# Kernel optimization log

Measured on AMD Instinct MI355X. Metric: run time of the kernel, lower is better.

Reference implementation:

```python
import jax, jax.numpy as jnp
import numpy as np

B, T, D, H = 128, 1024, 128, 512

def setup_inputs() -> dict:
    key = jax.random.key(0)
    ks = jax.random.split(key, 7)
    s = 1.0 / np.sqrt(H)
    return {
        "x":    jax.random.normal(ks[0], (B, T, D), dtype=jnp.float32),
        "W_ih": jax.random.uniform(ks[1], (4 * H, D), jnp.float32, -s, s),
        "W_hh": jax.random.uniform(ks[2], (4 * H, H), jnp.float32, -s, s),
        "b_ih": jax.random.uniform(ks[3], (4 * H,), jnp.float32, -s, s),
        "b_hh": jax.random.uniform(ks[4], (4 * H,), jnp.float32, -s, s),
        "W_fc": jax.random.uniform(ks[5], (1, H), jnp.float32, -s, s),
        "b_fc": jax.random.uniform(ks[6], (1,), jnp.float32, -s, s),
    }

def _lstm_last_hidden(x, W_ih, W_hh, b_ih, b_hh):
    # Precompute input-side gate projections for all timesteps: [T, B, 4H]
    xg = jnp.einsum('btd,gd->tbg', x, W_ih) + (b_ih + b_hh)
    Bq = x.shape[0]
    Hq = W_hh.shape[1]
    h0 = jnp.zeros((Bq, Hq), x.dtype)
    c0 = jnp.zeros((Bq, Hq), x.dtype)

    def step(carry, g_in):
        h, c = carry
        g = g_in + h @ W_hh.T                      # [B, 4H]
        i, f, gc, o = jnp.split(g, 4, axis=-1)     # PyTorch gate order i,f,g,o
        i = jax.nn.sigmoid(i)
        f = jax.nn.sigmoid(f)
        gc = jnp.tanh(gc)
        o = jax.nn.sigmoid(o)
        c = f * c + i * gc
        h = o * jnp.tanh(c)
        return (h, c), None

    (h_last, _), _ = jax.lax.scan(step, (h0, c0), xg)
    return h_last

def reference(x, W_ih, W_hh, b_ih, b_hh, W_fc, b_fc):
    h = _lstm_last_hidden(x, W_ih, W_hh, b_ih, b_hh)   # out[:, -1, :]
    return jax.nn.sigmoid(h @ W_fc.T + b_fc)           # [B, 1]
```

## Files before the change

kernel.cpp:

```cpp
#include <hip/hip_runtime.h>
#include <hip/hip_bf16.h>

#define Bsz 128
#define Tsz 1024
#define Dsz 128
#define Hsz 512
#define NBLK 256
#define NKC 20

typedef __attribute__((ext_vector_type(8))) short short8;
typedef __attribute__((ext_vector_type(4))) float f4;
typedef unsigned long long u64;

__device__ __forceinline__ short bf16_rne(float f) {
  unsigned u = __builtin_bit_cast(unsigned, f);
  u += 0x7fffu + ((u >> 16) & 1u);
  return (short)(u >> 16);
}
__device__ __forceinline__ float sigmoid_(float v) { return 1.f / (1.f + __expf(-v)); }

__global__ __launch_bounds__(256, 1) void lstm_persist(
    const float* __restrict__ x, const float* __restrict__ W_ih,
    const float* __restrict__ W_hh, const float* __restrict__ b_ih,
    const float* __restrict__ b_hh, const float* __restrict__ W_fc,
    const float* __restrict__ b_fc, float* __restrict__ out,
    int* flags, unsigned short* hb0, unsigned short* hb1)
{
  const int bx = blockIdx.x;
  const int bt = bx & 7, ks = bx >> 3;
  const int b0 = bt << 4, k0 = ks << 4;
  const int tx = threadIdx.x;
  const int wave = tx >> 6, lane = tx & 63;
  const int m = lane & 15, quad = lane >> 4;
  const int k_l = tx & 15, b_l = tx >> 4;

  __shared__ short8 A_lds[NKC][64];
  __shared__ f4 gates_lds[4][64];
  __shared__ float fc_red[16][16];

  int* gflags = flags + bt * 32;

  short8 wfrag[NKC];
  {
    const int j = wave * Hsz + k0 + m;
    #pragma unroll
    for (int kc = 0; kc < NKC; ++kc) {
      const int kk = kc * 32 + quad * 8;
      const float* src = (kk < Dsz) ? (W_ih + (size_t)j * Dsz + kk)
                                    : (W_hh + (size_t)j * Hsz + (kk - Dsz));
      const f4* sv = (const f4*)src;
      f4 v0 = sv[0], v1 = sv[1];
      short8 w;
      w[0] = bf16_rne(v0[0]); w[1] = bf16_rne(v0[1]);
      w[2] = bf16_rne(v0[2]); w[3] = bf16_rne(v0[3]);
      w[4] = bf16_rne(v1[0]); w[5] = bf16_rne(v1[1]);
      w[6] = bf16_rne(v1[2]); w[7] = bf16_rne(v1[3]);
      wfrag[kc] = w;
    }
  }
  float bias[4];
  #pragma unroll
  for (int g = 0; g < 4; ++g)
    bias[g] = b_ih[g * Hsz + k0 + k_l] + b_hh[g * Hsz + k0 + k_l];
  float c_reg = 0.f;

  for (int t = 0; t < Tsz; ++t) {
    unsigned short* hnext = (t & 1) ? hb1 : hb0;
    const unsigned short* hprev = (t & 1) ? hb0 : hb1;

    const f4* xv = (const f4*)(x + (size_t)(b0 + m) * (Tsz * Dsz)
                               + (size_t)t * Dsz + wave * 32 + quad * 8);
    f4 v0 = xv[0], v1 = xv[1];

    if (t > 0) {
      for (;;) {
        int f = __hip_atomic_load(gflags + (lane & 31),
                                  __ATOMIC_RELAXED, __HIP_MEMORY_SCOPE_AGENT);
        if (__all(f >= t)) break;
        __builtin_amdgcn_s_sleep(1);
      }
      #pragma unroll
      for (int q = 0; q < 4; ++q) {
        const int kc = 4 + wave * 4 + q;
        const int kh = (kc - 4) * 32 + quad * 8;
        const u64* p = (const u64*)(hprev + (size_t)(b0 + m) * Hsz + kh);
        u64 lo = __hip_atomic_load(p,     __ATOMIC_RELAXED, __HIP_MEMORY_SCOPE_AGENT);
        u64 hi = __hip_atomic_load(p + 1, __ATOMIC_RELAXED, __HIP_MEMORY_SCOPE_AGENT);
        u64* dst = (u64*)&A_lds[kc][lane];
        dst[0] = lo; dst[1] = hi;
      }
    } else {
      short8 z = {0, 0, 0, 0, 0, 0, 0, 0};
      #pragma unroll
      for (int q = 0; q < 4; ++q) A_lds[4 + wave * 4 + q][lane] = z;
    }

    {
      short8 a;
      a[0] = bf16_rne(v0[0]); a[1] = bf16_rne(v0[1]);
      a[2] = bf16_rne(v0[2]); a[3] = bf16_rne(v0[3]);
      a[4] = bf16_rne(v1[0]); a[5] = bf16_rne(v1[1]);
      a[6] = bf16_rne(v1[2]); a[7] = bf16_rne(v1[3]);
      A_lds[wave][lane] = a;
    }
    __syncthreads();

    f4 acc0 = {0.f, 0.f, 0.f, 0.f}, acc1 = {0.f, 0.f, 0.f, 0.f};
    #pragma unroll
    for (int kc = 0; kc < NKC; kc += 2) {
      acc0 = __builtin_amdgcn_mfma_f32_16x16x32_bf16(A_lds[kc][lane],     wfrag[kc],     acc0, 0, 0, 0);
      acc1 = __builtin_amdgcn_mfma_f32_16x16x32_bf16(A_lds[kc + 1][lane], wfrag[kc + 1], acc1, 0, 0, 0);
    }
    gates_lds[wave][lane] = acc0 + acc1;
    __syncthreads();

    {
      const int lp = ((b_l >> 2) << 4) + k_l;
      const int r = b_l & 3;
      float pi = gates_lds[0][lp][r] + bias[0];
      float pf = gates_lds[1][lp][r] + bias[1];
      float pg = gates_lds[2][lp][r] + bias[2];
      float po = gates_lds[3][lp][r] + bias[3];
      float iv = sigmoid_(pi), fv = sigmoid_(pf), ov = sigmoid_(po);
      float gv = tanhf(pg);
      c_reg = fv * c_reg + iv * gv;
      float hv = ov * tanhf(c_reg);
      unsigned hbits = (unsigned)(unsigned short)bf16_rne(hv);
      unsigned obits = __shfl_xor(hbits, 1);
      if ((k_l & 1) == 0) {
        unsigned packed = hbits | (obits << 16);
        unsigned* p = (unsigned*)(hnext + (size_t)(b0 + b_l) * Hsz + k0 + k_l);
        __hip_atomic_store(p, packed, __ATOMIC_RELAXED, __HIP_MEMORY_SCOPE_AGENT);
      }
    }
    __syncthreads();
    if (tx == 0)
      __hip_atomic_store(gflags + ks, t + 1, __ATOMIC_RELAXED, __HIP_MEMORY_SCOPE_AGENT);
  }

  if (ks == 0) {
    for (;;) {
      int f = __hip_atomic_load(gflags + (lane & 31),
                                __ATOMIC_RELAXED, __HIP_MEMORY_SCOPE_AGENT);
      if (__all(f >= Tsz)) break;
      __builtin_amdgcn_s_sleep(1);
    }
    const unsigned short* hl = hb1;
    const u64* p = (const u64*)(hl + (size_t)(b0 + b_l) * Hsz + k_l * 32);
    float partial = 0.f;
    #pragma unroll
    for (int q = 0; q < 8; ++q) {
      u64 v = __hip_atomic_load(p + q, __ATOMIC_RELAXED, __HIP_MEMORY_SCOPE_AGENT);
      #pragma unroll
      for (int e = 0; e < 4; ++e) {
        unsigned hv16 = (unsigned)((v >> (16 * e)) & 0xffffu);
        partial += __builtin_bit_cast(float, hv16 << 16) * W_fc[k_l * 32 + q * 4 + e];
      }
    }
    fc_red[b_l][k_l] = partial;
    __syncthreads();
    if (k_l == 0) {
      float s = b_fc[0];
      #pragma unroll
      for (int e = 0; e < 16; ++e) s += fc_red[b_l][e];
      out[b0 + b_l] = sigmoid_(s);
    }
  }
}

extern "C" void kernel_launch(void* const* d_in, const int* in_sizes, int n_in,
                              void* d_out, int out_size, void* d_ws, size_t ws_size,
                              hipStream_t stream) {
  const float* x    = (const float*)d_in[0];
  const float* W_ih = (const float*)d_in[1];
  const float* W_hh = (const float*)d_in[2];
  const float* b_ih = (const float*)d_in[3];
  const float* b_hh = (const float*)d_in[4];
  const float* W_fc = (const float*)d_in[5];
  const float* b_fc = (const float*)d_in[6];
  float* out = (float*)d_out;
  char* ws = (char*)d_ws;
  int* flags = (int*)ws;
  unsigned short* hb0 = (unsigned short*)(ws + 4096);
  unsigned short* hb1 = (unsigned short*)(ws + 4096 + (size_t)Bsz * Hsz * 2);
  hipMemsetAsync(ws, 0, 4096, stream);
  lstm_persist<<<NBLK, 256, 0, stream>>>(x, W_ih, W_hh, b_ih, b_hh, W_fc, b_fc,
                                         out, flags, hb0, hb1);
}
```

Baseline: 3.124 ms.

## Restructure LSTM step: gate-interleaved weights, shuffle gate exchange, padded flags, x prefetch

```diff
diff --git a/kernel.cpp b/kernel.cpp
--- a/kernel.cpp
+++ b/kernel.cpp
@@ -6,18 +6,24 @@
 #define Dsz 128
 #define Hsz 512
 #define NBLK 256
-#define NKC 20
+#define NXC 4
+#define NHC 16
 
 typedef __attribute__((ext_vector_type(8))) short short8;
 typedef __attribute__((ext_vector_type(4))) float f4;
 typedef unsigned long long u64;
 
-__device__ __forceinline__ short bf16_rne(float f) {
+__device__ __forceinline__ unsigned short bf16_rne(float f) {
   unsigned u = __builtin_bit_cast(unsigned, f);
   u += 0x7fffu + ((u >> 16) & 1u);
-  return (short)(u >> 16);
+  return (unsigned short)(u >> 16);
 }
 __device__ __forceinline__ float sigmoid_(float v) { return 1.f / (1.f + __expf(-v)); }
+__device__ __forceinline__ float tanh_(float v) {
+  v = fminf(fmaxf(v, -15.f), 15.f);
+  float e = __expf(2.f * v);
+  return (e - 1.f) / (e + 1.f);
+}
 
 __global__ __launch_bounds__(256, 1) void lstm_persist(
     const float* __restrict__ x, const float* __restrict__ W_ih,
@@ -32,19 +38,22 @@
   const int tx = threadIdx.x;
   const int wave = tx >> 6, lane = tx & 63;
   const int m = lane & 15, quad = lane >> 4;
-  const int k_l = tx & 15, b_l = tx >> 4;
-
-  __shared__ short8 A_lds[NKC][64];
-  __shared__ f4 gates_lds[4][64];
+  const int g_own = (lane >> 2) & 3, c_own = lane & 3;
+  const int mycol = k0 + wave * 4 + c_own;
+  const int myrow = b0 + quad * 4 + g_own;
+
+  __shared__ short8 A_x[2][NXC][64];
+  __shared__ short8 A_h[NHC][64];
   __shared__ float fc_red[16][16];
-
-  int* gflags = flags + bt * 32;
-
-  short8 wfrag[NKC];
+  __shared__ int token;
+
+  int* gflags = flags + bt * 1024;
+
+  short8 wfrag[NXC + NHC];
   {
-    const int j = wave * Hsz + k0 + m;
-    #pragma unroll
-    for (int kc = 0; kc < NKC; ++kc) {
+    const int j = g_own * Hsz + k0 + wave * 4 + c_own;
+    #pragma unroll
+    for (int kc = 0; kc < NXC + NHC; ++kc) {
       const int kk = kc * 32 + quad * 8;
       const float* src = (kk < Dsz) ? (W_ih + (size_t)j * Dsz + kk)
                                     : (W_hh + (size_t)j * Hsz + (kk - Dsz));
@@ -58,95 +67,127 @@
       wfrag[kc] = w;
     }
   }
-  float bias[4];
-  #pragma unroll
-  for (int g = 0; g < 4; ++g)
-    bias[g] = b_ih[g * Hsz + k0 + k_l] + b_hh[g * Hsz + k0 + k_l];
+  const float bias0 = b_ih[0 * Hsz + mycol] + b_hh[0 * Hsz + mycol];
+  const float bias1 = b_ih[1 * Hsz + mycol] + b_hh[1 * Hsz + mycol];
+  const float bias2 = b_ih[2 * Hsz + mycol] + b_hh[2 * Hsz + mycol];
+  const float bias3 = b_ih[3 * Hsz + mycol] + b_hh[3 * Hsz + mycol];
   float c_reg = 0.f;
+
+  {
+    const f4* xv = (const f4*)(x + (size_t)(b0 + m) * (Tsz * Dsz) + wave * 32 + quad * 8);
+    f4 v0 = xv[0], v1 = xv[1];
+    short8 a;
+    a[0] = bf16_rne(v0[0]); a[1] = bf16_rne(v0[1]);
+    a[2] = bf16_rne(v0[2]); a[3] = bf16_rne(v0[3]);
+    a[4] = bf16_rne(v1[0]); a[5] = bf16_rne(v1[1]);
+    a[6] = bf16_rne(v1[2]); a[7] = bf16_rne(v1[3]);
+    A_x[0][wave][lane] = a;
+    short8 z = {0, 0, 0, 0, 0, 0, 0, 0};
+    #pragma unroll
+    for (int q = 0; q < 4; ++q) A_h[wave * 4 + q][lane] = z;
+    if (tx == 0) token = 0;
+  }
 
   for (int t = 0; t < Tsz; ++t) {
     unsigned short* hnext = (t & 1) ? hb1 : hb0;
     const unsigned short* hprev = (t & 1) ? hb0 : hb1;
 
-    const f4* xv = (const f4*)(x + (size_t)(b0 + m) * (Tsz * Dsz)
-                               + (size_t)t * Dsz + wave * 32 + quad * 8);
-    f4 v0 = xv[0], v1 = xv[1];
-
     if (t > 0) {
-      for (;;) {
-        int f = __hip_atomic_load(gflags + (lane & 31),
-                                  __ATOMIC_RELAXED, __HIP_MEMORY_SCOPE_AGENT);
-        if (__all(f >= t)) break;
-        __builtin_amdgcn_s_sleep(1);
+      if (wave == 0) {
+        const int fi = (lane & 31) * 32;
+        for (;;) {
+          int f = __hip_atomic_load(gflags + fi, __ATOMIC_RELAXED, __HIP_MEMORY_SCOPE_AGENT);
+          if (__all(f >= t)) break;
+          __builtin_amdgcn_s_sleep(1);
+        }
+        __hip_atomic_store(&token, t, __ATOMIC_RELAXED, __HIP_MEMORY_SCOPE_WORKGROUP);
+      } else {
+        while (__hip_atomic_load(&token, __ATOMIC_RELAXED, __HIP_MEMORY_SCOPE_WORKGROUP) < t) {}
       }
       #pragma unroll
       for (int q = 0; q < 4; ++q) {
-        const int kc = 4 + wave * 4 + q;
-        const int kh = (kc - 4) * 32 + quad * 8;
-        const u64* p = (const u64*)(hprev + (size_t)(b0 + m) * Hsz + kh);
+        const int hc = wave * 4 + q;
+        const u64* p = (const u64*)(hprev + (size_t)(b0 + m) * Hsz + hc * 32 + quad * 8);
         u64 lo = __hip_atomic_load(p,     __ATOMIC_RELAXED, __HIP_MEMORY_SCOPE_AGENT);
         u64 hi = __hip_atomic_load(p + 1, __ATOMIC_RELAXED, __HIP_MEMORY_SCOPE_AGENT);
-        u64* dst = (u64*)&A_lds[kc][lane];
+        u64* dst = (u64*)&A_h[hc][lane];
         dst[0] = lo; dst[1] = hi;
       }
-    } else {
-      short8 z = {0, 0, 0, 0, 0, 0, 0, 0};
-      #pragma unroll
-      for (int q = 0; q < 4; ++q) A_lds[4 + wave * 4 + q][lane] = z;
-    }
-
-    {
+    }
+    __syncthreads();
+
+    const int xb = t & 1;
+    f4 acc0 = {0.f, 0.f, 0.f, 0.f}, acc1 = {0.f, 0.f, 0.f, 0.f};
+    acc0 = __builtin_amdgcn_mfma_f32_16x16x32_bf16(A_x[xb][0][lane], wfrag[0], acc0, 0, 0, 0);
+    acc1 = __builtin_amdgcn_mfma_f32_16x16x32_bf16(A_x[xb][1][lane], wfrag[1], acc1, 0, 0, 0);
+    acc0 = __builtin_amdgcn_mfma_f32_16x16x32_bf16(A_x[xb][2][lane], wfrag[2], acc0, 0, 0, 0);
+    acc1 = __builtin_amdgcn_mfma_f32_16x16x32_bf16(A_x[xb][3][lane], wfrag[3], acc1, 0, 0, 0);
+    #pragma unroll
+    for (int hc = 0; hc < NHC; hc += 2) {
+      acc0 = __builtin_amdgcn_mfma_f32_16x16x32_bf16(A_h[hc][lane],     wfrag[NXC + hc],     acc0, 0, 0, 0);
+      acc1 = __builtin_amdgcn_mfma_f32_16x16x32_bf16(A_h[hc + 1][lane], wfrag[NXC + hc + 1], acc1, 0, 0, 0);
+    }
+    f4 acc = acc0 + acc1;
+
+    float a01 = (g_own & 1) ? acc[1] : acc[0];
+    float a23 = (g_own & 1) ? acc[3] : acc[2];
+    float own = (g_own & 2) ? a23 : a01;
+    float b01 = (g_own & 1) ? acc[0] : acc[1];
+    float b23 = (g_own & 1) ? acc[2] : acc[3];
+    float s1 = (g_own & 2) ? b23 : b01;
+    float s2 = (g_own & 2) ? a01 : a23;
+    float s3 = (g_own & 2) ? b01 : b23;
+    float x4  = __shfl_xor(s1, 4);
+    float x8  = __shfl_xor(s2, 8);
+    float x12 = __shfl_xor(s3, 12);
+    #define PICK(e) ({ int _e = (e); float _lo = (_e & 1) ? x4 : own; \
+                       float _hi = (_e & 1) ? x12 : x8; (_e & 2) ? _hi : _lo; })
+    float pi = PICK(g_own)     + bias0;
+    float pf = PICK(g_own ^ 1) + bias1;
+    float pg = PICK(g_own ^ 2) + bias2;
+    float po = PICK(g_own ^ 3) + bias3;
+    #undef PICK
+    float iv = sigmoid_(pi), fv = sigmoid_(pf), ov = sigmoid_(po);
+    float gv = tanh_(pg);
+    c_reg = fv * c_reg + iv * gv;
+    float hv = ov * tanh_(c_reg);
+
+    float h1 = __shfl_xor(hv, 1);
+    float h2 = __shfl_xor(hv, 2);
+    float h3 = __shfl_xor(hv, 3);
+    if (c_own == 0) {
+      u64 packed = (u64)bf16_rne(hv) | ((u64)bf16_rne(h1) << 16)
+                 | ((u64)bf16_rne(h2) << 32) | ((u64)bf16_rne(h3) << 48);
+      u64* p = (u64*)(hnext + (size_t)myrow * Hsz + k0 + wave * 4);
+      __hip_atomic_store(p, packed, __ATOMIC_RELAXED, __HIP_MEMORY_SCOPE_AGENT);
+    }
+
+    if (t + 1 < Tsz) {
+      const f4* xv = (const f4*)(x + (size_t)(b0 + m) * (Tsz * Dsz)
+                                 + (size_t)(t + 1) * Dsz + wave * 32 + quad * 8);
+      f4 v0 = xv[0], v1 = xv[1];
       short8 a;
       a[0] = bf16_rne(v0[0]); a[1] = bf16_rne(v0[1]);
       a[2] = bf16_rne(v0[2]); a[3] = bf16_rne(v0[3]);
       a[4] = bf16_rne(v1[0]); a[5] = bf16_rne(v1[1]);
       a[6] = bf16_rne(v1[2]); a[7] = bf16_rne(v1[3]);
-      A_lds[wave][lane] = a;
-    }
-    __syncthreads();
-
-    f4 acc0 = {0.f, 0.f, 0.f, 0.f}, acc1 = {0.f, 0.f, 0.f, 0.f};
-    #pragma unroll
-    for (int kc = 0; kc < NKC; kc += 2) {
-      acc0 = __builtin_amdgcn_mfma_f32_16x16x32_bf16(A_lds[kc][lane],     wfrag[kc],     acc0, 0, 0, 0);
-      acc1 = __builtin_amdgcn_mfma_f32_16x16x32_bf16(A_lds[kc + 1][lane], wfrag[kc + 1], acc1, 0, 0, 0);
-    }
-    gates_lds[wave][lane] = acc0 + acc1;
-    __syncthreads();
-
-    {
-      const int lp = ((b_l >> 2) << 4) + k_l;
-      const int r = b_l & 3;
-      float pi = gates_lds[0][lp][r] + bias[0];
-      float pf = gates_lds[1][lp][r] + bias[1];
-      float pg = gates_lds[2][lp][r] + bias[2];
-      float po = gates_lds[3][lp][r] + bias[3];
-      float iv = sigmoid_(pi), fv = sigmoid_(pf), ov = sigmoid_(po);
-      float gv = tanhf(pg);
-      c_reg = fv * c_reg + iv * gv;
-      float hv = ov * tanhf(c_reg);
-      unsigned hbits = (unsigned)(unsigned short)bf16_rne(hv);
-      unsigned obits = __shfl_xor(hbits, 1);
-      if ((k_l & 1) == 0) {
-        unsigned packed = hbits | (obits << 16);
-        unsigned* p = (unsigned*)(hnext + (size_t)(b0 + b_l) * Hsz + k0 + k_l);
-        __hip_atomic_store(p, packed, __ATOMIC_RELAXED, __HIP_MEMORY_SCOPE_AGENT);
-      }
-    }
+      A_x[(t + 1) & 1][wave][lane] = a;
+    }
+
     __syncthreads();
     if (tx == 0)
-      __hip_atomic_store(gflags + ks, t + 1, __ATOMIC_RELAXED, __HIP_MEMORY_SCOPE_AGENT);
+      __hip_atomic_store(gflags + ks * 32, t + 1, __ATOMIC_RELAXED, __HIP_MEMORY_SCOPE_AGENT);
   }
 
   if (ks == 0) {
+    const int k_l = tx & 15, b_l = tx >> 4;
+    const int fi = (lane & 31) * 32;
     for (;;) {
-      int f = __hip_atomic_load(gflags + (lane & 31),
-                                __ATOMIC_RELAXED, __HIP_MEMORY_SCOPE_AGENT);
+      int f = __hip_atomic_load(gflags + fi, __ATOMIC_RELAXED, __HIP_MEMORY_SCOPE_AGENT);
       if (__all(f >= Tsz)) break;
       __builtin_amdgcn_s_sleep(1);
     }
-    const unsigned short* hl = hb1;
-    const u64* p = (const u64*)(hl + (size_t)(b0 + b_l) * Hsz + k_l * 32);
+    const u64* p = (const u64*)(hb1 + (size_t)(b0 + b_l) * Hsz + k_l * 32);
     float partial = 0.f;
     #pragma unroll
     for (int q = 0; q < 8; ++q) {
@@ -181,9 +222,9 @@
   float* out = (float*)d_out;
   char* ws = (char*)d_ws;
   int* flags = (int*)ws;
-  unsigned short* hb0 = (unsigned short*)(ws + 4096);
-  unsigned short* hb1 = (unsigned short*)(ws + 4096 + (size_t)Bsz * Hsz * 2);
-  hipMemsetAsync(ws, 0, 4096, stream);
+  unsigned short* hb0 = (unsigned short*)(ws + 65536);
+  unsigned short* hb1 = (unsigned short*)(ws + 65536 + (size_t)Bsz * Hsz * 2);
+  hipMemsetAsync(ws, 0, 32768, stream);
   lstm_persist<<<NBLK, 256, 0, stream>>>(x, W_ih, W_hh, b_ih, b_hh, W_fc, b_fc,
                                          out, flags, hb0, hb1);
 }
```

Measured after the change: 4.042 ms. +29.4%, slower.
